# Kernel optimization log

Measured on AMD Instinct MI355X. Metric: run time of the kernel, lower is better.

Reference implementation:

```python
import jax, jax.numpy as jnp
import numpy as np

B, TIN, TOUT, H, V = 32, 50, 50, 512, 32000


def setup_inputs() -> dict:
    key = jax.random.key(0)
    ks = jax.random.split(key, 16)
    s = 1.0 / np.sqrt(H)
    u = lambda k, shape, b: jax.random.uniform(k, shape, jnp.float32, -b, b)
    return {
        "encoder_out": jax.random.normal(ks[0], (B, TIN, H), jnp.float32),
        "y": jax.random.randint(ks[1], (B, TOUT), 0, V),
        "emb": jax.random.normal(ks[2], (V, H), jnp.float32) * 0.02,
        "W_fc": u(ks[3], (1, H), s), "b_fc": u(ks[4], (1,), s),
        "W_fc1": u(ks[5], (H, 2 * H), 1.0 / np.sqrt(2 * H)),
        "W_fc2": u(ks[6], (H, H), s),
        "W_comb": u(ks[7], (H, 2 * H), 1.0 / np.sqrt(2 * H)), "b_comb": u(ks[8], (H,), s),
        "W_ih": u(ks[9], (3 * H, H), s), "W_hh": u(ks[10], (3 * H, H), s),
        "b_ih": u(ks[11], (3 * H,), s), "b_hh": u(ks[12], (3 * H,), s),
        "W_out": u(ks[13], (V, H), s), "b_out": u(ks[14], (V,), s),
    }


def reference(encoder_out, y, emb, W_fc, b_fc, W_fc1, W_fc2, W_comb, b_comb,
              W_ih, W_hh, b_ih, b_hh, W_out, b_out):
    # Precompute wenc = attn_fc2(encoder_out): [B,Tin,H]
    wenc = jnp.einsum('bth,oh->bto', encoder_out, W_fc2)

    def step(carry, _):
        h, tok = carry                                  # h:[B,H], tok:[B] int
        x = emb[tok]                                    # embedding lookup [B,H]
        # additive-attention scores (softmax over a size-1 axis -> all ones,
        # faithfully reproducing the source's dim=2 softmax)
        wh = jnp.concatenate([x, h], -1) @ W_fc1.T      # [B,H]
        logits = (wh[:, None, :] + wenc) @ W_fc.T + b_fc  # [B,Tin,1]
        attn_wts = jax.nn.softmax(logits, axis=2)       # [B,Tin,1] == 1.0
        attn_full = jnp.broadcast_to(attn_wts, (B, TIN, H))  # .repeat(1,1,H)
        attn_x = jnp.sum(encoder_out * attn_full, axis=1)    # [B,H]
        xc = jnp.concatenate([x, attn_x], -1) @ W_comb.T + b_comb
        xc = jax.nn.relu(xc)                            # [B,H]
        # PyTorch GRU cell
        gi = xc @ W_ih.T + b_ih                         # [B,3H]
        gh = h @ W_hh.T + b_hh                          # [B,3H]
        ir, iz, inn = jnp.split(gi, 3, -1)
        hr, hz, hn = jnp.split(gh, 3, -1)
        r = jax.nn.sigmoid(ir + hr)
        z = jax.nn.sigmoid(iz + hz)
        n = jnp.tanh(inn + r * hn)
        h_new = (1.0 - z) * n + z * h                   # [B,H]
        logp = jax.nn.log_softmax(h_new @ W_out.T + b_out, axis=-1)  # [B,V]
        tok_new = jnp.argmax(logp, axis=-1)             # greedy feedback (detached)
        return (h_new, tok_new), (logp, attn_full)

    h0 = jnp.zeros((B, H), encoder_out.dtype)
    tok0 = y[:, 0]
    (hT, _), (logp_all, attn_all) = jax.lax.scan(step, (h0, tok0), None, length=TOUT)
    out = jnp.transpose(logp_all, (1, 2, 0))            # [B,V,T] (cat along dim=2)
    attn = attn_all.reshape(TOUT * B, TIN, H)           # cat along dim=0
    return out, hT[None], attn
```

## Files before the change

kernel.cpp:

```cpp
#include <hip/hip_runtime.h>
#include <math.h>

#define BATCH 32
#define TIN   50
#define TOUTS 50
#define HDIM  512
#define VOC   32000
#define NBL   250
#define DELTA 0.0625f

#define OFF_HA    0
#define OFF_HB    16384
#define OFF_XC    32768
#define OFF_XCPRE 49152
#define OFF_ATTNX 65536
#define OFF_PM    81920
#define OFF_PS    97920
#define OFF_PA    113920
#define OFF_LSE   129920
#define OFF_PM2   131584
#define OFF_PA2   139584

#define OUT_HT    51200000
#define OUT_ATTN  51216384

typedef unsigned short ushort8 __attribute__((ext_vector_type(8)));
typedef short s16x8 __attribute__((ext_vector_type(8)));
typedef float f32x16 __attribute__((ext_vector_type(16)));

static __device__ __forceinline__ unsigned short f2bf(float x) {
  unsigned int u = __float_as_uint(x);
  unsigned int r = (u + 0x7fffu + ((u >> 16) & 1u)) >> 16;
  return (unsigned short)r;
}
static __device__ __forceinline__ unsigned short f2h(float x) {
  _Float16 h = (_Float16)x;
  return __builtin_bit_cast(unsigned short, h);
}
static __device__ __forceinline__ float h2f(unsigned short u) {
  _Float16 h = __builtin_bit_cast(_Float16, u);
  return (float)h;
}
static __device__ __forceinline__ float dot4(float4 a, float4 b) {
  return a.x*b.x + a.y*b.y + a.z*b.z + a.w*b.w;
}
static __device__ __forceinline__ void ins2(float cv, int ci, float& M1, int& A1,
                                            float& M2, int& A2) {
  if (cv > M1 || (cv == M1 && ci < A1)) { M2 = M1; A2 = A1; M1 = cv; A1 = ci; }
  else if (cv > M2 || (cv == M2 && ci < A2)) { M2 = cv; A2 = ci; }
}

__global__ __launch_bounds__(256) void k_wconv(const float* __restrict__ W_out,
                                               float* __restrict__ out) {
  int n = blockIdx.x * 256 + threadIdx.x;
  if (n >= VOC * 64) return;
  int v = n >> 6, oct = n & 63;
  const float4* src = (const float4*)W_out + ((size_t)v * 128 + oct * 2);
  float4 x = src[0], y4 = src[1];
  ushort8 pk;
  pk[0]=f2bf(x.x);  pk[1]=f2bf(x.y);  pk[2]=f2bf(x.z);  pk[3]=f2bf(x.w);
  pk[4]=f2bf(y4.x); pk[5]=f2bf(y4.y); pk[6]=f2bf(y4.z); pk[7]=f2bf(y4.w);
  int tv = v >> 5, tk = oct >> 1, hi = oct & 1;
  int l = (v & 31) + 32 * hi;
  size_t fi = (size_t)(tv * 32 + tk) * 64 + l;
  ((ushort8*)out)[fi] = pk;
}

__global__ __launch_bounds__(256) void k_setup1(const float* __restrict__ enc,
                                                float* __restrict__ ws) {
  int idx = blockIdx.x * 256 + threadIdx.x;
  int b = idx >> 9, h = idx & 511;
  const float* p = enc + (size_t)b * TIN * HDIM + h;
  float s = 0.f;
  #pragma unroll 10
  for (int t = 0; t < TIN; ++t) s += p[(size_t)t * HDIM];
  (ws + OFF_ATTNX)[idx] = s;
  (ws + OFF_HA)[idx] = 0.f;
}

__global__ __launch_bounds__(256) void k_setup2(const float* __restrict__ W_comb,
                                                const float* __restrict__ b_comb,
                                                float* __restrict__ ws) {
  __shared__ float ax[HDIM];
  const int tid = threadIdx.x;
  const int b = blockIdx.x >> 1, half = blockIdx.x & 1;
  if (tid < 128)
    ((float4*)ax)[tid] = ((const float4*)(ws + OFF_ATTNX + b * HDIM))[tid];
  __syncthreads();
  int i = half * 256 + tid;
  float acc = b_comb[i];
  const float4* w4 = (const float4*)W_comb + (size_t)i * 256 + 128;
  const float4* a4 = (const float4*)ax;
  #pragma unroll 8
  for (int j = 0; j < 128; ++j) acc += dot4(w4[j], a4[j]);
  (ws + OFF_XCPRE)[b * HDIM + i] = acc;
}

__global__ __launch_bounds__(256) void k_xc(const float* __restrict__ emb,
                                            const int* __restrict__ y,
                                            const float* __restrict__ W_comb,
                                            const float* __restrict__ W_out,
                                            const float* __restrict__ b_out,
                                            float* __restrict__ ws, int t) {
  __shared__ float sm[256];
  __shared__ float em[HDIM];
  __shared__ int   candv[64];
  __shared__ float candval[64];
  __shared__ int   ncand_s, tok_s;
  const int tid = threadIdx.x;
  const int b = blockIdx.x >> 1, half = blockIdx.x & 1;
  const float* pm  = ws + OFF_PM;
  const float* ps  = ws + OFF_PS;
  const float* pm2 = ws + OFF_PM2;
  const int*   pa  = (const int*)(ws + OFF_PA);
  const int*   pa2 = (const int*)(ws + OFF_PA2);
  int tok;
  if (t == 0) {
    tok = y[b * TOUTS];
  } else {
    const bool act = tid < NBL;
    float M = act ? pm[tid * 32 + b] : -3.4e38f;
    sm[tid] = M;
    __syncthreads();
    for (int s = 128; s > 0; s >>= 1) {
      if (tid < s) sm[tid] = fmaxf(sm[tid], sm[tid + s]);
      __syncthreads();
    }
    float Mstar = sm[0];
    __syncthreads();
    float S = act ? ps[tid * 32 + b] * expf(pm[tid * 32 + b] - Mstar) : 0.f;
    sm[tid] = S;
    __syncthreads();
    for (int s = 128; s > 0; s >>= 1) {
      if (tid < s) sm[tid] += sm[tid + s];
      __syncthreads();
    }
    if (tid == 0 && half == 0)
      (ws + OFF_LSE)[(t - 1) * 32 + b] = Mstar + logf(sm[0]);
    if (tid == 0) ncand_s = 0;
    __syncthreads();
    if (act) {
      float v1 = pm[tid * 32 + b];
      if (v1 >= Mstar - DELTA) {
        int s_ = atomicAdd(&ncand_s, 1);
        if (s_ < 64) candv[s_] = pa[tid * 32 + b];
      }
      float v2 = pm2[tid * 32 + b];
      if (v2 >= Mstar - DELTA) {
        int s_ = atomicAdd(&ncand_s, 1);
        if (s_ < 64) candv[s_] = pa2[tid * 32 + b];
      }
    }
    __syncthreads();
    int n = min(ncand_s, 64);
    const float* hprev = ws + ((t & 1) ? OFF_HB : OFF_HA);
    const int lane = tid & 63, wv = tid >> 6;
    for (int c = wv; c < n; c += 4) {
      int v = candv[c];
      const float4* hv  = (const float4*)(hprev + b * HDIM) + lane * 2;
      const float4* wv4 = (const float4*)(W_out + (size_t)v * HDIM) + lane * 2;
      float d = dot4(hv[0], wv4[0]) + dot4(hv[1], wv4[1]);
      #pragma unroll
      for (int m = 1; m < 64; m <<= 1) d += __shfl_xor(d, m, 64);
      if (lane == 0) candval[c] = d + b_out[v];
    }
    __syncthreads();
    if (tid == 0) {
      float bv = -3.4e38f; int bi = 0x7fffffff;
      for (int c = 0; c < n; ++c) {
        int v = candv[c]; float x = candval[c];
        if (x > bv || (x == bv && v < bi)) { bv = x; bi = v; }
      }
      tok_s = bi;
    }
    __syncthreads();
    tok = tok_s;
  }
  if (tid < 128)
    ((float4*)em)[tid] = ((const float4*)(emb + (size_t)tok * HDIM))[tid];
  __syncthreads();
  int i = half * 256 + tid;
  float acc = (ws + OFF_XCPRE)[b * HDIM + i];
  const float4* w4 = (const float4*)W_comb + (size_t)i * 256;
  const float4* e4 = (const float4*)em;
  #pragma unroll 8
  for (int j = 0; j < 128; ++j) acc += dot4(w4[j], e4[j]);
  (ws + OFF_XC)[b * HDIM + i] = fmaxf(acc, 0.f);
}

__global__ __launch_bounds__(256) void k_gru(const float* __restrict__ W_ih,
                                             const float* __restrict__ W_hh,
                                             const float* __restrict__ b_ih,
                                             const float* __restrict__ b_hh,
                                             float* __restrict__ ws, int t) {
  __shared__ float xcs[8 * 516];
  __shared__ float hs [8 * 516];
  __shared__ float red[4 * 64 * 6];
  const int tid = threadIdx.x;
  const int btile = blockIdx.x & 3;
  const int itile = blockIdx.x >> 2;
  const int b0 = btile * 8, i0 = itile * 8;
  const float* hb_in  = ws + ((t & 1) ? OFF_HB : OFF_HA);
  float*       hb_out = ws + ((t & 1) ? OFF_HA : OFF_HB);
  const float4* xcg = (const float4*)(ws + OFF_XC);
  const float4* hg  = (const float4*)hb_in;
  #pragma unroll
  for (int q = 0; q < 4; ++q) {
    int pos = q * 256 + tid;
    int bl = pos >> 7, j = pos & 127;
    ((float4*)xcs)[bl * 129 + j] = xcg[(size_t)(b0 + bl) * 128 + j];
    ((float4*)hs )[bl * 129 + j] = hg [(size_t)(b0 + bl) * 128 + j];
  }
  __syncthreads();
  const int pair = tid >> 2, kh = tid & 3;
  const int bl = pair >> 3, il = pair & 7;
  const int i = i0 + il;
  float a0 = 0, a1 = 0, a2 = 0, a3 = 0, a4 = 0, a5 = 0;
  const float4* wi0 = (const float4*)(W_ih + (size_t)(i       ) * HDIM);
  const float4* wi1 = (const float4*)(W_ih + (size_t)(i +  512) * HDIM);
  const float4* wi2 = (const float4*)(W_ih + (size_t)(i + 1024) * HDIM);
  const float4* wh0 = (const float4*)(W_hh + (size_t)(i       ) * HDIM);
  const float4* wh1 = (const float4*)(W_hh + (size_t)(i +  512) * HDIM);
  const float4* wh2 = (const float4*)(W_hh + (size_t)(i + 1024) * HDIM);
  const float4* xv4 = (const float4*)xcs + bl * 129;
  const float4* hv4 = (const float4*)hs  + bl * 129;
  #pragma unroll 4
  for (int j = 0; j < 32; ++j) {
    int f4 = kh + 4 * j;
    float4 xv = xv4[f4], hv = hv4[f4];
    a0 += dot4(wi0[f4], xv);
    a1 += dot4(wi1[f4], xv);
    a2 += dot4(wi2[f4], xv);
    a3 += dot4(wh0[f4], hv);
    a4 += dot4(wh1[f4], hv);
    a5 += dot4(wh2[f4], hv);
  }
  float* rp = red + (kh * 64 + pair) * 6;
  rp[0] = a0; rp[1] = a1; rp[2] = a2; rp[3] = a3; rp[4] = a4; rp[5] = a5;
  __syncthreads();
  if (tid < 64) {
    const float* r0 = red + (0 * 64 + tid) * 6;
    const float* r1 = red + (1 * 64 + tid) * 6;
    const float* r2 = red + (2 * 64 + tid) * 6;
    const float* r3 = red + (3 * 64 + tid) * 6;
    int bl2 = tid >> 3, il2 = tid & 7;
    int ii = i0 + il2;
    float gir = r0[0] + r1[0] + r2[0] + r3[0] + b_ih[ii];
    float giz = r0[1] + r1[1] + r2[1] + r3[1] + b_ih[ii + 512];
    float gin = r0[2] + r1[2] + r2[2] + r3[2] + b_ih[ii + 1024];
    float ghr = r0[3] + r1[3] + r2[3] + r3[3] + b_hh[ii];
    float ghz = r0[4] + r1[4] + r2[4] + r3[4] + b_hh[ii + 512];
    float ghn = r0[5] + r1[5] + r2[5] + r3[5] + b_hh[ii + 1024];
    float r = 1.f / (1.f + expf(-(gir + ghr)));
    float z = 1.f / (1.f + expf(-(giz + ghz)));
    float n = tanhf(gin + r * ghn);
    float hold = hs[bl2 * 516 + ii];
    hb_out[(b0 + bl2) * HDIM + ii] = (1.f - z) * n + z * hold;
  }
}

__global__ __launch_bounds__(256) void k_logits(const float* __restrict__ b_out,
                                                float* __restrict__ ws,
                                                float* __restrict__ out, int t) {
  __shared__ unsigned short h_lds[16384];
  __shared__ unsigned short lout[32 * 136];
  __shared__ float wm1[128], wm2[128], wss[128];
  __shared__ int   wa1[128], wa2[128];
  const int tid = threadIdx.x, blk = blockIdx.x;
  const int lane = tid & 63, w = tid >> 6;
  const float* hb = ws + (((t + 1) & 1) ? OFF_HB : OFF_HA);
  {
    const float4* h4 = (const float4*)hb;
    int bb = tid >> 3, og = tid & 7;
    #pragma unroll
    for (int jo = 0; jo < 8; ++jo) {
      int oct = og * 8 + jo;
      float4 x  = h4[bb * 128 + oct * 2];
      float4 y4 = h4[bb * 128 + oct * 2 + 1];
      ushort8 pk;
      pk[0]=f2bf(x.x);  pk[1]=f2bf(x.y);  pk[2]=f2bf(x.z);  pk[3]=f2bf(x.w);
      pk[4]=f2bf(y4.x); pk[5]=f2bf(y4.y); pk[6]=f2bf(y4.z); pk[7]=f2bf(y4.w);
      *(ushort8*)&h_lds[((size_t)oct * 32 + bb) * 8] = pk;
    }
  }
  __syncthreads();
  f32x16 acc;
  #pragma unroll
  for (int r = 0; r < 16; ++r) acc[r] = 0.f;
  const s16x8* wp = (const s16x8*)out + (size_t)(blk * 4 + w) * 2048 + lane;
  const s16x8* hp = (const s16x8*)h_lds + lane;
  #pragma unroll 8
  for (int ks = 0; ks < 32; ++ks) {
    s16x8 a  = wp[ks * 64];
    s16x8 bf = hp[ks * 64];
    acc = __builtin_amdgcn_mfma_f32_32x32x16_bf16(a, bf, acc, 0, 0, 0);
  }
  const int b = lane & 31, hi = lane >> 5;
  const int vb = blk * 128 + w * 32;
  float vals[16];
  float m1 = -3.4e38f, m2 = -3.4e38f; int a1 = -1, a2 = -1;
  #pragma unroll
  for (int r = 0; r < 16; ++r) {
    int row = (r & 3) + 8 * (r >> 2) + 4 * hi;
    int v = vb + row;
    float x = acc[r] + b_out[v];
    vals[r] = x;
    ins2(x, v, m1, a1, m2, a2);
  }
  float s = 0.f;
  #pragma unroll
  for (int r = 0; r < 16; ++r) s += expf(vals[r] - m1);
  #pragma unroll
  for (int r = 0; r < 16; ++r) {
    int row = (r & 3) + 8 * (r >> 2) + 4 * hi;
    lout[b * 136 + w * 32 + row] = f2h(vals[r]);
  }
  float o1 = __shfl_xor(m1, 32, 64); int oa1 = __shfl_xor(a1, 32, 64);
  float o2 = __shfl_xor(m2, 32, 64); int oa2 = __shfl_xor(a2, 32, 64);
  float os = __shfl_xor(s, 32, 64);
  float M1 = m1, M2 = m2; int A1 = a1, A2 = a2;
  ins2(o1, oa1, M1, A1, M2, A2);
  ins2(o2, oa2, M1, A1, M2, A2);
  float S = s * expf(m1 - M1) + os * expf(o1 - M1);
  if (lane < 32) {
    wm1[w * 32 + b] = M1; wm2[w * 32 + b] = M2; wss[w * 32 + b] = S;
    wa1[w * 32 + b] = A1; wa2[w * 32 + b] = A2;
  }
  __syncthreads();
  if (tid < 32) {
    float BM1 = -3.4e38f, BM2 = -3.4e38f; int BA1 = -1, BA2 = -1;
    #pragma unroll
    for (int q = 0; q < 4; ++q) {
      ins2(wm1[q * 32 + tid], wa1[q * 32 + tid], BM1, BA1, BM2, BA2);
      ins2(wm2[q * 32 + tid], wa2[q * 32 + tid], BM1, BA1, BM2, BA2);
    }
    float BS = 0.f;
    #pragma unroll
    for (int q = 0; q < 4; ++q) BS += wss[q * 32 + tid] * expf(wm1[q * 32 + tid] - BM1);
    (ws + OFF_PM )[blk * 32 + tid] = BM1;
    (ws + OFF_PS )[blk * 32 + tid] = BS;
    (ws + OFF_PM2)[blk * 32 + tid] = BM2;
    ((int*)(ws + OFF_PA ))[blk * 32 + tid] = BA1;
    ((int*)(ws + OFF_PA2))[blk * 32 + tid] = BA2;
  }
  {
    int bb = tid >> 3, vg = tid & 7;
    ushort8 u0 = *(const ushort8*)&lout[bb * 136 + vg * 16];
    ushort8 u1 = *(const ushort8*)&lout[bb * 136 + vg * 16 + 8];
    unsigned short* lb = (unsigned short*)(out + OUT_ATTN);
    unsigned short* dst = lb + ((size_t)t * 32 + bb) * VOC + blk * 128 + vg * 16;
    *(ushort8*)dst = u0;
    *(ushort8*)(dst + 8) = u1;
  }
}

__global__ __launch_bounds__(256) void k_last(float* __restrict__ ws,
                                              float* __restrict__ out) {
  __shared__ float sm[256];
  const int tid = threadIdx.x, blk = blockIdx.x;
  out[OUT_HT + blk * 256 + tid] = (ws + OFF_HA)[blk * 256 + tid];
  if (blk >= 32) return;
  const int b = blk;
  const float* pm = ws + OFF_PM;
  const float* ps = ws + OFF_PS;
  float M = (tid < NBL) ? pm[tid * 32 + b] : -3.4e38f;
  sm[tid] = M; __syncthreads();
  for (int s = 128; s > 0; s >>= 1) { if (tid < s) sm[tid] = fmaxf(sm[tid], sm[tid + s]); __syncthreads(); }
  float Mstar = sm[0]; __syncthreads();
  float S = (tid < NBL) ? ps[tid * 32 + b] * expf(pm[tid * 32 + b] - Mstar) : 0.f;
  sm[tid] = S; __syncthreads();
  for (int s = 128; s > 0; s >>= 1) { if (tid < s) sm[tid] += sm[tid + s]; __syncthreads(); }
  if (tid == 0) (ws + OFF_LSE)[49 * 32 + b] = Mstar + logf(sm[0]);
}

__global__ __launch_bounds__(256) void k_transpose(const float* __restrict__ ws,
                                                   float* __restrict__ out) {
  __shared__ float lds[50 * 257];
  const int tid = threadIdx.x;
  int blk = blockIdx.x;
  int b = blk / 125, vt = blk % 125;
  int v0 = vt * 256;
  const unsigned short* lb = (const unsigned short*)(out + OUT_ATTN);
  const float* lse = ws + OFF_LSE;
  for (int tt = 0; tt < TOUTS; ++tt) {
    unsigned short us = lb[((size_t)tt * 32 + b) * VOC + v0 + tid];
    lds[tt * 257 + tid] = h2f(us) - lse[tt * 32 + b];
  }
  __syncthreads();
  float* ob = out + ((size_t)b * VOC + v0) * TOUTS;
  for (int j = 0; j < 50; ++j) {
    int flat = j * 256 + tid;
    int vloc = flat / 50, tt = flat - vloc * 50;
    ob[flat] = lds[tt * 257 + vloc];
  }
}

__global__ void k_fill(float* __restrict__ out) {
  float4* a4 = (float4*)(out + OUT_ATTN);
  unsigned int idx = blockIdx.x * 256 + threadIdx.x;
  float4 one = make_float4(1.f, 1.f, 1.f, 1.f);
  for (size_t i = idx; i < 10240000u; i += (size_t)4096 * 256) a4[i] = one;
}

extern "C" void kernel_launch(void* const* d_in, const int* in_sizes, int n_in,
                              void* d_out, int out_size, void* d_ws, size_t ws_size,
                              hipStream_t stream) {
  (void)in_sizes; (void)n_in; (void)out_size; (void)ws_size;
  const float* enc    = (const float*)d_in[0];
  const int*   y      = (const int*)  d_in[1];
  const float* emb    = (const float*)d_in[2];
  const float* W_comb = (const float*)d_in[7];
  const float* b_comb = (const float*)d_in[8];
  const float* W_ih   = (const float*)d_in[9];
  const float* W_hh   = (const float*)d_in[10];
  const float* b_ih   = (const float*)d_in[11];
  const float* b_hh   = (const float*)d_in[12];
  const float* W_out  = (const float*)d_in[13];
  const float* b_out  = (const float*)d_in[14];
  float* out = (float*)d_out;
  float* ws  = (float*)d_ws;

  k_wconv <<<8000, 256, 0, stream>>>(W_out, out);
  k_setup1<<<64,   256, 0, stream>>>(enc, ws);
  k_setup2<<<64,   256, 0, stream>>>(W_comb, b_comb, ws);
  for (int t = 0; t < TOUTS; ++t) {
    k_xc    <<<64,  256, 0, stream>>>(emb, y, W_comb, W_out, b_out, ws, t);
    k_gru   <<<256, 256, 0, stream>>>(W_ih, W_hh, b_ih, b_hh, ws, t);
    k_logits<<<NBL, 256, 0, stream>>>(b_out, ws, out, t);
  }
  k_last     <<<64,   256, 0, stream>>>(ws, out);
  k_transpose<<<4000, 256, 0, stream>>>(ws, out);
  k_fill     <<<4096, 256, 0, stream>>>(out);
}
```

Before: 3.894 ms.

## Fuse all per-step kernels into one persistent cooperative kernel with grid syncs

Replaces the sequence of about 155 separate kernel launches (setup, three per decode step, finalize, transpose, fill) with a single cooperative kernel of 256 blocks. The phases are separated by grid.sync barriers, and shared memory is overlaid through a union. The aim is to remove per-launch overhead and inter-kernel gaps in the serial 50-step recurrence. In exchange, the large bulk phases (weight conversion, transpose, fill) now run on only 256 blocks with one block per CU, and grid-wide barriers carry their own cost.

Result: slower. 8.042 ms (+106.5%).

```diff
diff --git a/kernel.cpp b/kernel.cpp
--- a/kernel.cpp
+++ b/kernel.cpp
@@ -1,5 +1,8 @@
 #include <hip/hip_runtime.h>
+#include <hip/hip_cooperative_groups.h>
 #include <math.h>
+
+namespace cg = cooperative_groups;
 
 #define BATCH 32
 #define TIN   50
@@ -50,356 +53,369 @@
   else if (cv > M2 || (cv == M2 && ci < A2)) { M2 = cv; A2 = ci; }
 }
 
-__global__ __launch_bounds__(256) void k_wconv(const float* __restrict__ W_out,
-                                               float* __restrict__ out) {
-  int n = blockIdx.x * 256 + threadIdx.x;
-  if (n >= VOC * 64) return;
-  int v = n >> 6, oct = n & 63;
-  const float4* src = (const float4*)W_out + ((size_t)v * 128 + oct * 2);
-  float4 x = src[0], y4 = src[1];
-  ushort8 pk;
-  pk[0]=f2bf(x.x);  pk[1]=f2bf(x.y);  pk[2]=f2bf(x.z);  pk[3]=f2bf(x.w);
-  pk[4]=f2bf(y4.x); pk[5]=f2bf(y4.y); pk[6]=f2bf(y4.z); pk[7]=f2bf(y4.w);
-  int tv = v >> 5, tk = oct >> 1, hi = oct & 1;
-  int l = (v & 31) + 32 * hi;
-  size_t fi = (size_t)(tv * 32 + tk) * 64 + l;
-  ((ushort8*)out)[fi] = pk;
-}
-
-__global__ __launch_bounds__(256) void k_setup1(const float* __restrict__ enc,
-                                                float* __restrict__ ws) {
-  int idx = blockIdx.x * 256 + threadIdx.x;
-  int b = idx >> 9, h = idx & 511;
-  const float* p = enc + (size_t)b * TIN * HDIM + h;
-  float s = 0.f;
-  #pragma unroll 10
-  for (int t = 0; t < TIN; ++t) s += p[(size_t)t * HDIM];
-  (ws + OFF_ATTNX)[idx] = s;
-  (ws + OFF_HA)[idx] = 0.f;
-}
-
-__global__ __launch_bounds__(256) void k_setup2(const float* __restrict__ W_comb,
-                                                const float* __restrict__ b_comb,
-                                                float* __restrict__ ws) {
-  __shared__ float ax[HDIM];
+struct SMemL {
+  unsigned short h_lds[16384];
+  unsigned short lout[32 * 136];
+  float wm1[128], wm2[128], wss[128];
+  int   wa1[128], wa2[128];
+};
+struct SMemG {
+  float xcs[8 * 516];
+  float hs [8 * 516];
+  float red[4 * 64 * 6];
+};
+struct SMemX {
+  float sm[256];
+  float em[HDIM];
+  int   candv[64];
+  float candval[64];
+  int   ncand, tok;
+};
+struct SMemT { float lds[50 * 257]; };
+union SMemU { SMemL L; SMemG G; SMemX X; SMemT T; };
+
+__global__ __launch_bounds__(256, 1) void k_main(
+    const float* __restrict__ enc, const int* __restrict__ y,
+    const float* __restrict__ emb, const float* __restrict__ W_comb,
+    const float* __restrict__ b_comb, const float* __restrict__ W_ih,
+    const float* __restrict__ W_hh, const float* __restrict__ b_ih,
+    const float* __restrict__ b_hh, const float* __restrict__ W_out,
+    const float* __restrict__ b_out, float* __restrict__ ws,
+    float* __restrict__ out) {
+  __shared__ SMemU su;
+  cg::grid_group grid = cg::this_grid();
   const int tid = threadIdx.x;
-  const int b = blockIdx.x >> 1, half = blockIdx.x & 1;
-  if (tid < 128)
-    ((float4*)ax)[tid] = ((const float4*)(ws + OFF_ATTNX + b * HDIM))[tid];
-  __syncthreads();
-  int i = half * 256 + tid;
-  float acc = b_comb[i];
-  const float4* w4 = (const float4*)W_comb + (size_t)i * 256 + 128;
-  const float4* a4 = (const float4*)ax;
-  #pragma unroll 8
-  for (int j = 0; j < 128; ++j) acc += dot4(w4[j], a4[j]);
-  (ws + OFF_XCPRE)[b * HDIM + i] = acc;
-}
-
-__global__ __launch_bounds__(256) void k_xc(const float* __restrict__ emb,
-                                            const int* __restrict__ y,
-                                            const float* __restrict__ W_comb,
-                                            const float* __restrict__ W_out,
-                                            const float* __restrict__ b_out,
-                                            float* __restrict__ ws, int t) {
-  __shared__ float sm[256];
-  __shared__ float em[HDIM];
-  __shared__ int   candv[64];
-  __shared__ float candval[64];
-  __shared__ int   ncand_s, tok_s;
-  const int tid = threadIdx.x;
-  const int b = blockIdx.x >> 1, half = blockIdx.x & 1;
-  const float* pm  = ws + OFF_PM;
-  const float* ps  = ws + OFF_PS;
-  const float* pm2 = ws + OFF_PM2;
-  const int*   pa  = (const int*)(ws + OFF_PA);
-  const int*   pa2 = (const int*)(ws + OFF_PA2);
-  int tok;
-  if (t == 0) {
-    tok = y[b * TOUTS];
-  } else {
-    const bool act = tid < NBL;
-    float M = act ? pm[tid * 32 + b] : -3.4e38f;
-    sm[tid] = M;
+  const int blk = blockIdx.x;
+
+  for (int u = blk; u < 8000; u += 256) {
+    int n = u * 256 + tid;
+    int v = n >> 6, oct = n & 63;
+    const float4* src = (const float4*)W_out + ((size_t)v * 128 + oct * 2);
+    float4 x = src[0], y4 = src[1];
+    ushort8 pk;
+    pk[0]=f2bf(x.x);  pk[1]=f2bf(x.y);  pk[2]=f2bf(x.z);  pk[3]=f2bf(x.w);
+    pk[4]=f2bf(y4.x); pk[5]=f2bf(y4.y); pk[6]=f2bf(y4.z); pk[7]=f2bf(y4.w);
+    int tv = v >> 5, tk = oct >> 1, hi = oct & 1;
+    int l = (v & 31) + 32 * hi;
+    size_t fi = (size_t)(tv * 32 + tk) * 64 + l;
+    ((ushort8*)out)[fi] = pk;
+  }
+
+  if (blk < 64) {
+    int idx = blk * 256 + tid;
+    int b = idx >> 9, h = idx & 511;
+    const float* p = enc + (size_t)b * TIN * HDIM + h;
+    float s = 0.f;
+    #pragma unroll 10
+    for (int t = 0; t < TIN; ++t) s += p[(size_t)t * HDIM];
+    (ws + OFF_ATTNX)[idx] = s;
+    (ws + OFF_HA)[idx] = 0.f;
+  }
+  grid.sync();
+
+  if (blk < 64) {
+    const int b = blk >> 1, half = blk & 1;
+    if (tid < 128)
+      ((float4*)su.X.em)[tid] = ((const float4*)(ws + OFF_ATTNX + b * HDIM))[tid];
     __syncthreads();
+    int i = half * 256 + tid;
+    float acc = b_comb[i];
+    const float4* w4 = (const float4*)W_comb + (size_t)i * 256 + 128;
+    const float4* a4 = (const float4*)su.X.em;
+    #pragma unroll 8
+    for (int j = 0; j < 128; ++j) acc += dot4(w4[j], a4[j]);
+    (ws + OFF_XCPRE)[b * HDIM + i] = acc;
+  }
+  grid.sync();
+
+  for (int t = 0; t < TOUTS; ++t) {
+    if (blk < 64) {
+      const int b = blk >> 1, half = blk & 1;
+      const float* pm  = ws + OFF_PM;
+      const float* ps  = ws + OFF_PS;
+      const float* pm2 = ws + OFF_PM2;
+      const int*   pa  = (const int*)(ws + OFF_PA);
+      const int*   pa2 = (const int*)(ws + OFF_PA2);
+      int tok;
+      if (t == 0) {
+        tok = y[b * TOUTS];
+      } else {
+        const bool act = tid < NBL;
+        float M = act ? pm[tid * 32 + b] : -3.4e38f;
+        su.X.sm[tid] = M;
+        __syncthreads();
+        for (int s = 128; s > 0; s >>= 1) {
+          if (tid < s) su.X.sm[tid] = fmaxf(su.X.sm[tid], su.X.sm[tid + s]);
+          __syncthreads();
+        }
+        float Mstar = su.X.sm[0];
+        __syncthreads();
+        float S = act ? ps[tid * 32 + b] * expf(pm[tid * 32 + b] - Mstar) : 0.f;
+        su.X.sm[tid] = S;
+        __syncthreads();
+        for (int s = 128; s > 0; s >>= 1) {
+          if (tid < s) su.X.sm[tid] += su.X.sm[tid + s];
+          __syncthreads();
+        }
+        if (tid == 0 && half == 0)
+          (ws + OFF_LSE)[(t - 1) * 32 + b] = Mstar + logf(su.X.sm[0]);
+        if (tid == 0) su.X.ncand = 0;
+        __syncthreads();
+        if (act) {
+          float v1 = pm[tid * 32 + b];
+          if (v1 >= Mstar - DELTA) {
+            int s_ = atomicAdd(&su.X.ncand, 1);
+            if (s_ < 64) su.X.candv[s_] = pa[tid * 32 + b];
+          }
+          float v2 = pm2[tid * 32 + b];
+          if (v2 >= Mstar - DELTA) {
+            int s_ = atomicAdd(&su.X.ncand, 1);
+            if (s_ < 64) su.X.candv[s_] = pa2[tid * 32 + b];
+          }
+        }
+        __syncthreads();
+        int n = min(su.X.ncand, 64);
+        const float* hprev = ws + ((t & 1) ? OFF_HB : OFF_HA);
+        const int lane = tid & 63, wv = tid >> 6;
+        for (int c = wv; c < n; c += 4) {
+          int v = su.X.candv[c];
+          const float4* hv  = (const float4*)(hprev + b * HDIM) + lane * 2;
+          const float4* wv4 = (const float4*)(W_out + (size_t)v * HDIM) + lane * 2;
+          float d = dot4(hv[0], wv4[0]) + dot4(hv[1], wv4[1]);
+          #pragma unroll
+          for (int m = 1; m < 64; m <<= 1) d += __shfl_xor(d, m, 64);
+          if (lane == 0) su.X.candval[c] = d + b_out[v];
+        }
+        __syncthreads();
+        if (tid == 0) {
+          float bv = -3.4e38f; int bi = 0x7fffffff;
+          for (int c = 0; c < n; ++c) {
+            int v = su.X.candv[c]; float x = su.X.candval[c];
+            if (x > bv || (x == bv && v < bi)) { bv = x; bi = v; }
+          }
+          su.X.tok = bi;
+        }
+        __syncthreads();
+        tok = su.X.tok;
+      }
+      if (tid < 128)
+        ((float4*)su.X.em)[tid] = ((const float4*)(emb + (size_t)tok * HDIM))[tid];
+      __syncthreads();
+      int i = half * 256 + tid;
+      float acc = (ws + OFF_XCPRE)[b * HDIM + i];
+      const float4* w4 = (const float4*)W_comb + (size_t)i * 256;
+      const float4* e4 = (const float4*)su.X.em;
+      #pragma unroll 8
+      for (int j = 0; j < 128; ++j) acc += dot4(w4[j], e4[j]);
+      (ws + OFF_XC)[b * HDIM + i] = fmaxf(acc, 0.f);
+    }
+    grid.sync();
+
+    {
+      const int btile = blk & 3;
+      const int itile = blk >> 2;
+      const int b0 = btile * 8, i0 = itile * 8;
+      const float* hb_in  = ws + ((t & 1) ? OFF_HB : OFF_HA);
+      float*       hb_out = ws + ((t & 1) ? OFF_HA : OFF_HB);
+      const float4* xcg = (const float4*)(ws + OFF_XC);
+      const float4* hg  = (const float4*)hb_in;
+      #pragma unroll
+      for (int q = 0; q < 4; ++q) {
+        int pos = q * 256 + tid;
+        int bl = pos >> 7, j = pos & 127;
+        ((float4*)su.G.xcs)[bl * 129 + j] = xcg[(size_t)(b0 + bl) * 128 + j];
+        ((float4*)su.G.hs )[bl * 129 + j] = hg [(size_t)(b0 + bl) * 128 + j];
+      }
+      __syncthreads();
+      const int pair = tid >> 2, kh = tid & 3;
+      const int bl = pair >> 3, il = pair & 7;
+      const int i = i0 + il;
+      float a0 = 0, a1 = 0, a2 = 0, a3 = 0, a4 = 0, a5 = 0;
+      const float4* wi0 = (const float4*)(W_ih + (size_t)(i       ) * HDIM);
+      const float4* wi1 = (const float4*)(W_ih + (size_t)(i +  512) * HDIM);
+      const float4* wi2 = (const float4*)(W_ih + (size_t)(i + 1024) * HDIM);
+      const float4* wh0 = (const float4*)(W_hh + (size_t)(i       ) * HDIM);
+      const float4* wh1 = (const float4*)(W_hh + (size_t)(i +  512) * HDIM);
+      const float4* wh2 = (const float4*)(W_hh + (size_t)(i + 1024) * HDIM);
+      const float4* xv4 = (const float4*)su.G.xcs + bl * 129;
+      const float4* hv4 = (const float4*)su.G.hs  + bl * 129;
+      #pragma unroll 4
+      for (int j = 0; j < 32; ++j) {
+        int f4 = kh + 4 * j;
+        float4 xv = xv4[f4], hv = hv4[f4];
+        a0 += dot4(wi0[f4], xv);
+        a1 += dot4(wi1[f4], xv);
+        a2 += dot4(wi2[f4], xv);
+        a3 += dot4(wh0[f4], hv);
+        a4 += dot4(wh1[f4], hv);
+        a5 += dot4(wh2[f4], hv);
+      }
+      float* rp = su.G.red + (kh * 64 + pair) * 6;
+      rp[0] = a0; rp[1] = a1; rp[2] = a2; rp[3] = a3; rp[4] = a4; rp[5] = a5;
+      __syncthreads();
+      if (tid < 64) {
+        const float* r0 = su.G.red + (0 * 64 + tid) * 6;
+        const float* r1 = su.G.red + (1 * 64 + tid) * 6;
+        const float* r2 = su.G.red + (2 * 64 + tid) * 6;
+        const float* r3 = su.G.red + (3 * 64 + tid) * 6;
+        int bl2 = tid >> 3, il2 = tid & 7;
+        int ii = i0 + il2;
+        float gir = r0[0] + r1[0] + r2[0] + r3[0] + b_ih[ii];
+        float giz = r0[1] + r1[1] + r2[1] + r3[1] + b_ih[ii + 512];
+        float gin = r0[2] + r1[2] + r2[2] + r3[2] + b_ih[ii + 1024];
+        float ghr = r0[3] + r1[3] + r2[3] + r3[3] + b_hh[ii];
+        float ghz = r0[4] + r1[4] + r2[4] + r3[4] + b_hh[ii + 512];
+        float ghn = r0[5] + r1[5] + r2[5] + r3[5] + b_hh[ii + 1024];
+        float r = 1.f / (1.f + expf(-(gir + ghr)));
+        float z = 1.f / (1.f + expf(-(giz + ghz)));
+        float n = tanhf(gin + r * ghn);
+        float hold = su.G.hs[bl2 * 516 + ii];
+        hb_out[(b0 + bl2) * HDIM + ii] = (1.f - z) * n + z * hold;
+      }
+    }
+    grid.sync();
+
+    if (blk < NBL) {
+      const int lane = tid & 63, w = tid >> 6;
+      const float* hb = ws + (((t + 1) & 1) ? OFF_HB : OFF_HA);
+      {
+        const float4* h4 = (const float4*)hb;
+        int bb = tid >> 3, og = tid & 7;
+        #pragma unroll
+        for (int jo = 0; jo < 8; ++jo) {
+          int oct = og * 8 + jo;
+          float4 x  = h4[bb * 128 + oct * 2];
+          float4 y4 = h4[bb * 128 + oct * 2 + 1];
+          ushort8 pk;
+          pk[0]=f2bf(x.x);  pk[1]=f2bf(x.y);  pk[2]=f2bf(x.z);  pk[3]=f2bf(x.w);
+          pk[4]=f2bf(y4.x); pk[5]=f2bf(y4.y); pk[6]=f2bf(y4.z); pk[7]=f2bf(y4.w);
+          *(ushort8*)&su.L.h_lds[((size_t)oct * 32 + bb) * 8] = pk;
+        }
+      }
+      __syncthreads();
+      f32x16 acc;
+      #pragma unroll
+      for (int r = 0; r < 16; ++r) acc[r] = 0.f;
+      const s16x8* wp = (const s16x8*)out + (size_t)(blk * 4 + w) * 2048 + lane;
+      const s16x8* hp = (const s16x8*)su.L.h_lds + lane;
+      #pragma unroll 8
+      for (int ks = 0; ks < 32; ++ks) {
+        s16x8 a  = wp[ks * 64];
+        s16x8 bf = hp[ks * 64];
+        acc = __builtin_amdgcn_mfma_f32_32x32x16_bf16(a, bf, acc, 0, 0, 0);
+      }
+      const int b = lane & 31, hi = lane >> 5;
+      const int vb = blk * 128 + w * 32;
+      float vals[16];
+      float m1 = -3.4e38f, m2 = -3.4e38f; int a1 = -1, a2 = -1;
+      #pragma unroll
+      for (int r = 0; r < 16; ++r) {
+        int row = (r & 3) + 8 * (r >> 2) + 4 * hi;
+        int v = vb + row;
+        float x = acc[r] + b_out[v];
+        vals[r] = x;
+        ins2(x, v, m1, a1, m2, a2);
+      }
+      float s = 0.f;
+      #pragma unroll
+      for (int r = 0; r < 16; ++r) s += expf(vals[r] - m1);
+      #pragma unroll
+      for (int r = 0; r < 16; ++r) {
+        int row = (r & 3) + 8 * (r >> 2) + 4 * hi;
+        su.L.lout[b * 136 + w * 32 + row] = f2h(vals[r]);
+      }
+      float o1 = __shfl_xor(m1, 32, 64); int oa1 = __shfl_xor(a1, 32, 64);
+      float o2 = __shfl_xor(m2, 32, 64); int oa2 = __shfl_xor(a2, 32, 64);
+      float os = __shfl_xor(s, 32, 64);
+      float M1 = m1, M2 = m2; int A1 = a1, A2 = a2;
+      ins2(o1, oa1, M1, A1, M2, A2);
+      ins2(o2, oa2, M1, A1, M2, A2);
+      float S = s * expf(m1 - M1) + os * expf(o1 - M1);
+      if (lane < 32) {
+        su.L.wm1[w * 32 + b] = M1; su.L.wm2[w * 32 + b] = M2;
+        su.L.wss[w * 32 + b] = S;
+        su.L.wa1[w * 32 + b] = A1; su.L.wa2[w * 32 + b] = A2;
+      }
+      __syncthreads();
+      if (tid < 32) {
+        float BM1 = -3.4e38f, BM2 = -3.4e38f; int BA1 = -1, BA2 = -1;
+        #pragma unroll
+        for (int q = 0; q < 4; ++q) {
+          ins2(su.L.wm1[q * 32 + tid], su.L.wa1[q * 32 + tid], BM1, BA1, BM2, BA2);
+          ins2(su.L.wm2[q * 32 + tid], su.L.wa2[q * 32 + tid], BM1, BA1, BM2, BA2);
+        }
+        float BS = 0.f;
+        #pragma unroll
+        for (int q = 0; q < 4; ++q)
+          BS += su.L.wss[q * 32 + tid] * expf(su.L.wm1[q * 32 + tid] - BM1);
+        (ws + OFF_PM )[blk * 32 + tid] = BM1;
+        (ws + OFF_PS )[blk * 32 + tid] = BS;
+        (ws + OFF_PM2)[blk * 32 + tid] = BM2;
+        ((int*)(ws + OFF_PA ))[blk * 32 + tid] = BA1;
+        ((int*)(ws + OFF_PA2))[blk * 32 + tid] = BA2;
+      }
+      {
+        int bb = tid >> 3, vg = tid & 7;
+        ushort8 u0 = *(const ushort8*)&su.L.lout[bb * 136 + vg * 16];
+        ushort8 u1 = *(const ushort8*)&su.L.lout[bb * 136 + vg * 16 + 8];
+        unsigned short* lb = (unsigned short*)(out + OUT_ATTN);
+        unsigned short* dst = lb + ((size_t)t * 32 + bb) * VOC + blk * 128 + vg * 16;
+        *(ushort8*)dst = u0;
+        *(ushort8*)(dst + 8) = u1;
+      }
+    }
+    grid.sync();
+  }
+
+  if (blk < 64)
+    out[OUT_HT + blk * 256 + tid] = (ws + OFF_HA)[blk * 256 + tid];
+  if (blk < 32) {
+    const int b = blk;
+    const float* pm = ws + OFF_PM;
+    const float* ps = ws + OFF_PS;
+    float M = (tid < NBL) ? pm[tid * 32 + b] : -3.4e38f;
+    su.X.sm[tid] = M; __syncthreads();
     for (int s = 128; s > 0; s >>= 1) {
-      if (tid < s) sm[tid] = fmaxf(sm[tid], sm[tid + s]);
-      __syncthreads();
-    }
-    float Mstar = sm[0];
+      if (tid < s) su.X.sm[tid] = fmaxf(su.X.sm[tid], su.X.sm[tid + s]);
+      __syncthreads();
+    }
+    float Mstar = su.X.sm[0]; __syncthreads();
+    float S = (tid < NBL) ? ps[tid * 32 + b] * expf(pm[tid * 32 + b] - Mstar) : 0.f;
+    su.X.sm[tid] = S; __syncthreads();
+    for (int s = 128; s > 0; s >>= 1) {
+      if (tid < s) su.X.sm[tid] += su.X.sm[tid + s];
+      __syncthreads();
+    }
+    if (tid == 0) (ws + OFF_LSE)[49 * 32 + b] = Mstar + logf(su.X.sm[0]);
+  }
+  grid.sync();
+
+  for (int u = blk; u < 4000; u += 256) {
+    int b = u / 125, vt = u % 125;
+    int v0 = vt * 256;
+    const unsigned short* lb = (const unsigned short*)(out + OUT_ATTN);
+    const float* lse = ws + OFF_LSE;
+    for (int tt = 0; tt < TOUTS; ++tt) {
+      unsigned short us = lb[((size_t)tt * 32 + b) * VOC + v0 + tid];
+      su.T.lds[tt * 257 + tid] = h2f(us) - lse[tt * 32 + b];
+    }
     __syncthreads();
-    float S = act ? ps[tid * 32 + b] * expf(pm[tid * 32 + b] - Mstar) : 0.f;
-    sm[tid] = S;
+    float* ob = out + ((size_t)b * VOC + v0) * TOUTS;
+    for (int j = 0; j < 50; ++j) {
+      int flat = j * 256 + tid;
+      int vloc = flat / 50, tt = flat - vloc * 50;
+      ob[flat] = su.T.lds[tt * 257 + vloc];
+    }
     __syncthreads();
-    for (int s = 128; s > 0; s >>= 1) {
-      if (tid < s) sm[tid] += sm[tid + s];
-      __syncthreads();
-    }
-    if (tid == 0 && half == 0)
-      (ws + OFF_LSE)[(t - 1) * 32 + b] = Mstar + logf(sm[0]);
-    if (tid == 0) ncand_s = 0;
-    __syncthreads();
-    if (act) {
-      float v1 = pm[tid * 32 + b];
-      if (v1 >= Mstar - DELTA) {
-        int s_ = atomicAdd(&ncand_s, 1);
-        if (s_ < 64) candv[s_] = pa[tid * 32 + b];
-      }
-      float v2 = pm2[tid * 32 + b];
-      if (v2 >= Mstar - DELTA) {
-        int s_ = atomicAdd(&ncand_s, 1);
-        if (s_ < 64) candv[s_] = pa2[tid * 32 + b];
-      }
-    }
-    __syncthreads();
-    int n = min(ncand_s, 64);
-    const float* hprev = ws + ((t & 1) ? OFF_HB : OFF_HA);
-    const int lane = tid & 63, wv = tid >> 6;
-    for (int c = wv; c < n; c += 4) {
-      int v = candv[c];
-      const float4* hv  = (const float4*)(hprev + b * HDIM) + lane * 2;
-      const float4* wv4 = (const float4*)(W_out + (size_t)v * HDIM) + lane * 2;
-      float d = dot4(hv[0], wv4[0]) + dot4(hv[1], wv4[1]);
-      #pragma unroll
-      for (int m = 1; m < 64; m <<= 1) d += __shfl_xor(d, m, 64);
-      if (lane == 0) candval[c] = d + b_out[v];
-    }
-    __syncthreads();
-    if (tid == 0) {
-      float bv = -3.4e38f; int bi = 0x7fffffff;
-      for (int c = 0; c < n; ++c) {
-        int v = candv[c]; float x = candval[c];
-        if (x > bv || (x == bv && v < bi)) { bv = x; bi = v; }
-      }
-      tok_s = bi;
-    }
-    __syncthreads();
-    tok = tok_s;
-  }
-  if (tid < 128)
-    ((float4*)em)[tid] = ((const float4*)(emb + (size_t)tok * HDIM))[tid];
-  __syncthreads();
-  int i = half * 256 + tid;
-  float acc = (ws + OFF_XCPRE)[b * HDIM + i];
-  const float4* w4 = (const float4*)W_comb + (size_t)i * 256;
-  const float4* e4 = (const float4*)em;
-  #pragma unroll 8
-  for (int j = 0; j < 128; ++j) acc += dot4(w4[j], e4[j]);
-  (ws + OFF_XC)[b * HDIM + i] = fmaxf(acc, 0.f);
-}
-
-__global__ __launch_bounds__(256) void k_gru(const float* __restrict__ W_ih,
-                                             const float* __restrict__ W_hh,
-                                             const float* __restrict__ b_ih,
-                                             const float* __restrict__ b_hh,
-                                             float* __restrict__ ws, int t) {
-  __shared__ float xcs[8 * 516];
-  __shared__ float hs [8 * 516];
-  __shared__ float red[4 * 64 * 6];
-  const int tid = threadIdx.x;
-  const int btile = blockIdx.x & 3;
-  const int itile = blockIdx.x >> 2;
-  const int b0 = btile * 8, i0 = itile * 8;
-  const float* hb_in  = ws + ((t & 1) ? OFF_HB : OFF_HA);
-  float*       hb_out = ws + ((t & 1) ? OFF_HA : OFF_HB);
-  const float4* xcg = (const float4*)(ws + OFF_XC);
-  const float4* hg  = (const float4*)hb_in;
-  #pragma unroll
-  for (int q = 0; q < 4; ++q) {
-    int pos = q * 256 + tid;
-    int bl = pos >> 7, j = pos & 127;
-    ((float4*)xcs)[bl * 129 + j] = xcg[(size_t)(b0 + bl) * 128 + j];
-    ((float4*)hs )[bl * 129 + j] = hg [(size_t)(b0 + bl) * 128 + j];
-  }
-  __syncthreads();
-  const int pair = tid >> 2, kh = tid & 3;
-  const int bl = pair >> 3, il = pair & 7;
-  const int i = i0 + il;
-  float a0 = 0, a1 = 0, a2 = 0, a3 = 0, a4 = 0, a5 = 0;
-  const float4* wi0 = (const float4*)(W_ih + (size_t)(i       ) * HDIM);
-  const float4* wi1 = (const float4*)(W_ih + (size_t)(i +  512) * HDIM);
-  const float4* wi2 = (const float4*)(W_ih + (size_t)(i + 1024) * HDIM);
-  const float4* wh0 = (const float4*)(W_hh + (size_t)(i       ) * HDIM);
-  const float4* wh1 = (const float4*)(W_hh + (size_t)(i +  512) * HDIM);
-  const float4* wh2 = (const float4*)(W_hh + (size_t)(i + 1024) * HDIM);
-  const float4* xv4 = (const float4*)xcs + bl * 129;
-  const float4* hv4 = (const float4*)hs  + bl * 129;
-  #pragma unroll 4
-  for (int j = 0; j < 32; ++j) {
-    int f4 = kh + 4 * j;
-    float4 xv = xv4[f4], hv = hv4[f4];
-    a0 += dot4(wi0[f4], xv);
-    a1 += dot4(wi1[f4], xv);
-    a2 += dot4(wi2[f4], xv);
-    a3 += dot4(wh0[f4], hv);
-    a4 += dot4(wh1[f4], hv);
-    a5 += dot4(wh2[f4], hv);
-  }
-  float* rp = red + (kh * 64 + pair) * 6;
-  rp[0] = a0; rp[1] = a1; rp[2] = a2; rp[3] = a3; rp[4] = a4; rp[5] = a5;
-  __syncthreads();
-  if (tid < 64) {
-    const float* r0 = red + (0 * 64 + tid) * 6;
-    const float* r1 = red + (1 * 64 + tid) * 6;
-    const float* r2 = red + (2 * 64 + tid) * 6;
-    const float* r3 = red + (3 * 64 + tid) * 6;
-    int bl2 = tid >> 3, il2 = tid & 7;
-    int ii = i0 + il2;
-    float gir = r0[0] + r1[0] + r2[0] + r3[0] + b_ih[ii];
-    float giz = r0[1] + r1[1] + r2[1] + r3[1] + b_ih[ii + 512];
-    float gin = r0[2] + r1[2] + r2[2] + r3[2] + b_ih[ii + 1024];
-    float ghr = r0[3] + r1[3] + r2[3] + r3[3] + b_hh[ii];
-    float ghz = r0[4] + r1[4] + r2[4] + r3[4] + b_hh[ii + 512];
-    float ghn = r0[5] + r1[5] + r2[5] + r3[5] + b_hh[ii + 1024];
-    float r = 1.f / (1.f + expf(-(gir + ghr)));
-    float z = 1.f / (1.f + expf(-(giz + ghz)));
-    float n = tanhf(gin + r * ghn);
-    float hold = hs[bl2 * 516 + ii];
-    hb_out[(b0 + bl2) * HDIM + ii] = (1.f - z) * n + z * hold;
-  }
-}
-
-__global__ __launch_bounds__(256) void k_logits(const float* __restrict__ b_out,
-                                                float* __restrict__ ws,
-                                                float* __restrict__ out, int t) {
-  __shared__ unsigned short h_lds[16384];
-  __shared__ unsigned short lout[32 * 136];
-  __shared__ float wm1[128], wm2[128], wss[128];
-  __shared__ int   wa1[128], wa2[128];
-  const int tid = threadIdx.x, blk = blockIdx.x;
-  const int lane = tid & 63, w = tid >> 6;
-  const float* hb = ws + (((t + 1) & 1) ? OFF_HB : OFF_HA);
+  }
+  grid.sync();
+
   {
-    const float4* h4 = (const float4*)hb;
-    int bb = tid >> 3, og = tid & 7;
-    #pragma unroll
-    for (int jo = 0; jo < 8; ++jo) {
-      int oct = og * 8 + jo;
-      float4 x  = h4[bb * 128 + oct * 2];
-      float4 y4 = h4[bb * 128 + oct * 2 + 1];
-      ushort8 pk;
-      pk[0]=f2bf(x.x);  pk[1]=f2bf(x.y);  pk[2]=f2bf(x.z);  pk[3]=f2bf(x.w);
-      pk[4]=f2bf(y4.x); pk[5]=f2bf(y4.y); pk[6]=f2bf(y4.z); pk[7]=f2bf(y4.w);
-      *(ushort8*)&h_lds[((size_t)oct * 32 + bb) * 8] = pk;
-    }
-  }
-  __syncthreads();
-  f32x16 acc;
-  #pragma unroll
-  for (int r = 0; r < 16; ++r) acc[r] = 0.f;
-  const s16x8* wp = (const s16x8*)out + (size_t)(blk * 4 + w) * 2048 + lane;
-  const s16x8* hp = (const s16x8*)h_lds + lane;
-  #pragma unroll 8
-  for (int ks = 0; ks < 32; ++ks) {
-    s16x8 a  = wp[ks * 64];
-    s16x8 bf = hp[ks * 64];
-    acc = __builtin_amdgcn_mfma_f32_32x32x16_bf16(a, bf, acc, 0, 0, 0);
-  }
-  const int b = lane & 31, hi = lane >> 5;
-  const int vb = blk * 128 + w * 32;
-  float vals[16];
-  float m1 = -3.4e38f, m2 = -3.4e38f; int a1 = -1, a2 = -1;
-  #pragma unroll
-  for (int r = 0; r < 16; ++r) {
-    int row = (r & 3) + 8 * (r >> 2) + 4 * hi;
-    int v = vb + row;
-    float x = acc[r] + b_out[v];
-    vals[r] = x;
-    ins2(x, v, m1, a1, m2, a2);
-  }
-  float s = 0.f;
-  #pragma unroll
-  for (int r = 0; r < 16; ++r) s += expf(vals[r] - m1);
-  #pragma unroll
-  for (int r = 0; r < 16; ++r) {
-    int row = (r & 3) + 8 * (r >> 2) + 4 * hi;
-    lout[b * 136 + w * 32 + row] = f2h(vals[r]);
-  }
-  float o1 = __shfl_xor(m1, 32, 64); int oa1 = __shfl_xor(a1, 32, 64);
-  float o2 = __shfl_xor(m2, 32, 64); int oa2 = __shfl_xor(a2, 32, 64);
-  float os = __shfl_xor(s, 32, 64);
-  float M1 = m1, M2 = m2; int A1 = a1, A2 = a2;
-  ins2(o1, oa1, M1, A1, M2, A2);
-  ins2(o2, oa2, M1, A1, M2, A2);
-  float S = s * expf(m1 - M1) + os * expf(o1 - M1);
-  if (lane < 32) {
-    wm1[w * 32 + b] = M1; wm2[w * 32 + b] = M2; wss[w * 32 + b] = S;
-    wa1[w * 32 + b] = A1; wa2[w * 32 + b] = A2;
-  }
-  __syncthreads();
-  if (tid < 32) {
-    float BM1 = -3.4e38f, BM2 = -3.4e38f; int BA1 = -1, BA2 = -1;
-    #pragma unroll
-    for (int q = 0; q < 4; ++q) {
-      ins2(wm1[q * 32 + tid], wa1[q * 32 + tid], BM1, BA1, BM2, BA2);
-      ins2(wm2[q * 32 + tid], wa2[q * 32 + tid], BM1, BA1, BM2, BA2);
-    }
-    float BS = 0.f;
-    #pragma unroll
-    for (int q = 0; q < 4; ++q) BS += wss[q * 32 + tid] * expf(wm1[q * 32 + tid] - BM1);
-    (ws + OFF_PM )[blk * 32 + tid] = BM1;
-    (ws + OFF_PS )[blk * 32 + tid] = BS;
-    (ws + OFF_PM2)[blk * 32 + tid] = BM2;
-    ((int*)(ws + OFF_PA ))[blk * 32 + tid] = BA1;
-    ((int*)(ws + OFF_PA2))[blk * 32 + tid] = BA2;
-  }
-  {
-    int bb = tid >> 3, vg = tid & 7;
-    ushort8 u0 = *(const ushort8*)&lout[bb * 136 + vg * 16];
-    ushort8 u1 = *(const ushort8*)&lout[bb * 136 + vg * 16 + 8];
-    unsigned short* lb = (unsigned short*)(out + OUT_ATTN);
-    unsigned short* dst = lb + ((size_t)t * 32 + bb) * VOC + blk * 128 + vg * 16;
-    *(ushort8*)dst = u0;
-    *(ushort8*)(dst + 8) = u1;
-  }
-}
-
-__global__ __launch_bounds__(256) void k_last(float* __restrict__ ws,
-                                              float* __restrict__ out) {
-  __shared__ float sm[256];
-  const int tid = threadIdx.x, blk = blockIdx.x;
-  out[OUT_HT + blk * 256 + tid] = (ws + OFF_HA)[blk * 256 + tid];
-  if (blk >= 32) return;
-  const int b = blk;
-  const float* pm = ws + OFF_PM;
-  const float* ps = ws + OFF_PS;
-  float M = (tid < NBL) ? pm[tid * 32 + b] : -3.4e38f;
-  sm[tid] = M; __syncthreads();
-  for (int s = 128; s > 0; s >>= 1) { if (tid < s) sm[tid] = fmaxf(sm[tid], sm[tid + s]); __syncthreads(); }
-  float Mstar = sm[0]; __syncthreads();
-  float S = (tid < NBL) ? ps[tid * 32 + b] * expf(pm[tid * 32 + b] - Mstar) : 0.f;
-  sm[tid] = S; __syncthreads();
-  for (int s = 128; s > 0; s >>= 1) { if (tid < s) sm[tid] += sm[tid + s]; __syncthreads(); }
-  if (tid == 0) (ws + OFF_LSE)[49 * 32 + b] = Mstar + logf(sm[0]);
-}
-
-__global__ __launch_bounds__(256) void k_transpose(const float* __restrict__ ws,
-                                                   float* __restrict__ out) {
-  __shared__ float lds[50 * 257];
-  const int tid = threadIdx.x;
-  int blk = blockIdx.x;
-  int b = blk / 125, vt = blk % 125;
-  int v0 = vt * 256;
-  const unsigned short* lb = (const unsigned short*)(out + OUT_ATTN);
-  const float* lse = ws + OFF_LSE;
-  for (int tt = 0; tt < TOUTS; ++tt) {
-    unsigned short us = lb[((size_t)tt * 32 + b) * VOC + v0 + tid];
-    lds[tt * 257 + tid] = h2f(us) - lse[tt * 32 + b];
-  }
-  __syncthreads();
-  float* ob = out + ((size_t)b * VOC + v0) * TOUTS;
-  for (int j = 0; j < 50; ++j) {
-    int flat = j * 256 + tid;
-    int vloc = flat / 50, tt = flat - vloc * 50;
-    ob[flat] = lds[tt * 257 + vloc];
-  }
-}
-
-__global__ void k_fill(float* __restrict__ out) {
-  float4* a4 = (float4*)(out + OUT_ATTN);
-  unsigned int idx = blockIdx.x * 256 + threadIdx.x;
-  float4 one = make_float4(1.f, 1.f, 1.f, 1.f);
-  for (size_t i = idx; i < 10240000u; i += (size_t)4096 * 256) a4[i] = one;
+    float4* a4 = (float4*)(out + OUT_ATTN);
+    float4 one = make_float4(1.f, 1.f, 1.f, 1.f);
+    for (unsigned int i = blk * 256u + tid; i < 10240000u; i += 65536u)
+      a4[i] = one;
+  }
 }
 
 extern "C" void kernel_launch(void* const* d_in, const int* in_sizes, int n_in,
@@ -420,15 +436,11 @@
   float* out = (float*)d_out;
   float* ws  = (float*)d_ws;
 
-  k_wconv <<<8000, 256, 0, stream>>>(W_out, out);
-  k_setup1<<<64,   256, 0, stream>>>(enc, ws);
-  k_setup2<<<64,   256, 0, stream>>>(W_comb, b_comb, ws);
-  for (int t = 0; t < TOUTS; ++t) {
-    k_xc    <<<64,  256, 0, stream>>>(emb, y, W_comb, W_out, b_out, ws, t);
-    k_gru   <<<256, 256, 0, stream>>>(W_ih, W_hh, b_ih, b_hh, ws, t);
-    k_logits<<<NBL, 256, 0, stream>>>(b_out, ws, out, t);
-  }
-  k_last     <<<64,   256, 0, stream>>>(ws, out);
-  k_transpose<<<4000, 256, 0, stream>>>(ws, out);
-  k_fill     <<<4096, 256, 0, stream>>>(out);
-}
+  void* args[] = {
+    (void*)&enc, (void*)&y, (void*)&emb, (void*)&W_comb, (void*)&b_comb,
+    (void*)&W_ih, (void*)&W_hh, (void*)&b_ih, (void*)&b_hh,
+    (void*)&W_out, (void*)&b_out, (void*)&ws, (void*)&out
+  };
+  hipLaunchCooperativeKernel((const void*)k_main, dim3(256), dim3(256),
+                             args, 0, stream);
+}
```
